# Kernel optimization log

Measured on AMD Instinct MI355X. Metric: run time of the kernel, lower is better.

The kernel has to match this reference:

```python
import jax, jax.numpy as jnp
import numpy as np

N_HEADS = 16
D_K = 64
D_V = 64
HIDDEN = 1024
B, S = 2, 2048
LN_EPS = 1e-5


def setup_inputs() -> dict:
    key = jax.random.key(0)
    ks = jax.random.split(key, 6)
    inputs = jax.random.normal(ks[0], (B, S, HIDDEN), dtype=jnp.float32)
    attn_mask = jax.random.randint(ks[1], (B, S, S), 0, 2, dtype=jnp.int32)
    scale = 1.0 / np.sqrt(HIDDEN)
    W_Q = jax.random.normal(ks[2], (HIDDEN, HIDDEN), dtype=jnp.float32) * scale
    W_K = jax.random.normal(ks[3], (HIDDEN, HIDDEN), dtype=jnp.float32) * scale
    W_V = jax.random.normal(ks[4], (HIDDEN, HIDDEN), dtype=jnp.float32) * scale
    W_O = jax.random.normal(ks[5], (HIDDEN, HIDDEN), dtype=jnp.float32) * scale
    return {"inputs": inputs, "attn_mask": attn_mask,
            "W_Q": W_Q, "W_K": W_K, "W_V": W_V, "W_O": W_O}


def reference(inputs, attn_mask, W_Q, W_K, W_V, W_O):
    b, s, _ = inputs.shape
    # nn.Linear(bias=False): x @ W.T ; reshape to [B, H, S, d]
    Q = (inputs @ W_Q.T).reshape(b, s, N_HEADS, D_K).transpose(0, 2, 1, 3)
    K = (inputs @ W_K.T).reshape(b, s, N_HEADS, D_K).transpose(0, 2, 1, 3)
    V = (inputs @ W_V.T).reshape(b, s, N_HEADS, D_V).transpose(0, 2, 1, 3)
    scores = jnp.einsum('bhqd,bhkd->bhqk', Q, K) / np.sqrt(D_K)
    mask = (attn_mask == 0)[:, None, :, :]  # broadcast over heads
    scores = jnp.where(mask, jnp.float32(-1e9), scores)
    attn = jax.nn.softmax(scores, axis=-1)
    context = jnp.einsum('bhqk,bhkd->bhqd', attn, V)
    context = context.transpose(0, 2, 1, 3).reshape(b, s, N_HEADS * D_V)
    output = context @ W_O.T
    x = output + inputs  # residual
    # LayerNorm with default weight=1, bias=0, eps=1e-5
    mu = jnp.mean(x, axis=-1, keepdims=True)
    var = jnp.mean(jnp.square(x - mu), axis=-1, keepdims=True)
    out = (x - mu) * jax.lax.rsqrt(var + LN_EPS)
    return out, attn
```

## Files before the change

kernel.cpp:

```cpp
#include <hip/hip_runtime.h>

typedef unsigned short u16;
typedef __bf16 bf16x8 __attribute__((ext_vector_type(8)));
typedef float f32x4 __attribute__((ext_vector_type(4)));

static __device__ __forceinline__ u16 f32_to_bf16(float f) {
    unsigned u = __builtin_bit_cast(unsigned, f);
    u += 0x7fffu + ((u >> 16) & 1u);
    return (u16)(u >> 16);
}
static __device__ __forceinline__ float bf16_to_f32(u16 v) {
    return __builtin_bit_cast(float, ((unsigned)v) << 16);
}

__global__ __launch_bounds__(256) void cast_f32_bf16(const float* __restrict__ in,
                                                     u16* __restrict__ out, int n)
{
    int i = (blockIdx.x * 256 + threadIdx.x) * 4;
    if (i >= n) return;
    float4 v = *reinterpret_cast<const float4*>(in + i);
    ushort4 o;
    o.x = f32_to_bf16(v.x); o.y = f32_to_bf16(v.y);
    o.z = f32_to_bf16(v.z); o.w = f32_to_bf16(v.w);
    *reinterpret_cast<ushort4*>(out + i) = o;
}

__global__ __launch_bounds__(256) void gemm_abt_bf16(
    const u16* __restrict__ A, const u16* __restrict__ B,
    u16* __restrict__ C, int M, int N, int K)
{
    __shared__ __align__(16) u16 As[64][40];
    __shared__ __align__(16) u16 Bs[64][40];
    const int tid  = threadIdx.x;
    const int wave = tid >> 6, lane = tid & 63;
    const int quad = lane >> 4, l16 = lane & 15;
    const int m0 = blockIdx.y * 64, n0 = blockIdx.x * 64;

    f32x4 acc[4] = {};
    const int lr = tid >> 2;
    const int lc = (tid & 3) * 8;
    const u16* Ap = A + (size_t)(m0 + lr) * K + lc;
    const u16* Bp = B + (size_t)(n0 + lr) * K + lc;

    for (int k0 = 0; k0 < K; k0 += 32) {
        __syncthreads();
        *reinterpret_cast<int4*>(&As[lr][lc]) = *reinterpret_cast<const int4*>(Ap + k0);
        *reinterpret_cast<int4*>(&Bs[lr][lc]) = *reinterpret_cast<const int4*>(Bp + k0);
        __syncthreads();
        bf16x8 a = *reinterpret_cast<const bf16x8*>(&As[wave * 16 + l16][quad * 8]);
#pragma unroll
        for (int cb = 0; cb < 4; ++cb) {
            bf16x8 b = *reinterpret_cast<const bf16x8*>(&Bs[cb * 16 + l16][quad * 8]);
            acc[cb] = __builtin_amdgcn_mfma_f32_16x16x32_bf16(a, b, acc[cb], 0, 0, 0);
        }
    }
#pragma unroll
    for (int cb = 0; cb < 4; ++cb)
#pragma unroll
        for (int r = 0; r < 4; ++r) {
            int row = m0 + wave * 16 + quad * 4 + r;
            int col = n0 + cb * 16 + l16;
            C[(size_t)row * N + col] = f32_to_bf16(acc[cb][r]);
        }
}

__global__ __launch_bounds__(256) void gemm_abt_res_f32(
    const u16* __restrict__ A, const u16* __restrict__ B,
    const float* __restrict__ X, float* __restrict__ C, int M, int N, int K)
{
    __shared__ __align__(16) u16 As[64][40];
    __shared__ __align__(16) u16 Bs[64][40];
    const int tid  = threadIdx.x;
    const int wave = tid >> 6, lane = tid & 63;
    const int quad = lane >> 4, l16 = lane & 15;
    const int m0 = blockIdx.y * 64, n0 = blockIdx.x * 64;

    f32x4 acc[4] = {};
    const int lr = tid >> 2;
    const int lc = (tid & 3) * 8;
    const u16* Ap = A + (size_t)(m0 + lr) * K + lc;
    const u16* Bp = B + (size_t)(n0 + lr) * K + lc;

    for (int k0 = 0; k0 < K; k0 += 32) {
        __syncthreads();
        *reinterpret_cast<int4*>(&As[lr][lc]) = *reinterpret_cast<const int4*>(Ap + k0);
        *reinterpret_cast<int4*>(&Bs[lr][lc]) = *reinterpret_cast<const int4*>(Bp + k0);
        __syncthreads();
        bf16x8 a = *reinterpret_cast<const bf16x8*>(&As[wave * 16 + l16][quad * 8]);
#pragma unroll
        for (int cb = 0; cb < 4; ++cb) {
            bf16x8 b = *reinterpret_cast<const bf16x8*>(&Bs[cb * 16 + l16][quad * 8]);
            acc[cb] = __builtin_amdgcn_mfma_f32_16x16x32_bf16(a, b, acc[cb], 0, 0, 0);
        }
    }
#pragma unroll
    for (int cb = 0; cb < 4; ++cb)
#pragma unroll
        for (int r = 0; r < 4; ++r) {
            int row = m0 + wave * 16 + quad * 4 + r;
            int col = n0 + cb * 16 + l16;
            C[(size_t)row * N + col] = acc[cb][r] + X[(size_t)row * N + col];
        }
}

__global__ __launch_bounds__(256) void attn_kernel(
    const u16* __restrict__ Q, const u16* __restrict__ K,
    const u16* __restrict__ V, const int* __restrict__ mask,
    float* __restrict__ attn_out, u16* __restrict__ ctx_out)
{
    constexpr int S = 2048, HID = 1024, NH = 16;
    __shared__ __align__(16) u16 Qs[64][72];
    __shared__ __align__(16) u16 Ks[64][72];
    __shared__ __align__(16) u16 Vt[64][72];
    __shared__ __align__(16) u16 Ps[64][72];

    const int tid  = threadIdx.x;
    const int wave = tid >> 6, lane = tid & 63;
    const int quad = lane >> 4, l16 = lane & 15;
    const int qt = blockIdx.x, h = blockIdx.y, b = blockIdx.z;
    const size_t qkv_base = (size_t)b * S * HID + h * 64;

    const int lr = tid >> 2;
    const int lc = (tid & 3) * 16;
    {
        const u16* p = Q + qkv_base + (size_t)(qt * 64 + lr) * HID + lc;
        *reinterpret_cast<int4*>(&Qs[lr][lc])     = *reinterpret_cast<const int4*>(p);
        *reinterpret_cast<int4*>(&Qs[lr][lc + 8]) = *reinterpret_cast<const int4*>(p + 8);
    }

    float m_i[4], l_i[4];
#pragma unroll
    for (int r = 0; r < 4; ++r) { m_i[r] = -1e30f; l_i[r] = 0.f; }

    const int q_row0 = qt * 64 + wave * 16 + quad * 4;
    const size_t mask_b = (size_t)b * S * S;

    for (int kt = 0; kt < S / 64; ++kt) {
        __syncthreads();
        {
            const u16* p = K + qkv_base + (size_t)(kt * 64 + lr) * HID + lc;
            *reinterpret_cast<int4*>(&Ks[lr][lc])     = *reinterpret_cast<const int4*>(p);
            *reinterpret_cast<int4*>(&Ks[lr][lc + 8]) = *reinterpret_cast<const int4*>(p + 8);
        }
        __syncthreads();
        f32x4 sc[4] = {};
#pragma unroll
        for (int ks = 0; ks < 2; ++ks) {
            bf16x8 a = *reinterpret_cast<const bf16x8*>(&Qs[wave * 16 + l16][ks * 32 + quad * 8]);
#pragma unroll
            for (int cb = 0; cb < 4; ++cb) {
                bf16x8 bb = *reinterpret_cast<const bf16x8*>(&Ks[cb * 16 + l16][ks * 32 + quad * 8]);
                sc[cb] = __builtin_amdgcn_mfma_f32_16x16x32_bf16(a, bb, sc[cb], 0, 0, 0);
            }
        }
        float s_val[4][4];
#pragma unroll
        for (int cb = 0; cb < 4; ++cb) {
            int kcol = kt * 64 + cb * 16 + l16;
#pragma unroll
            for (int r = 0; r < 4; ++r) {
                int q = q_row0 + r;
                int mv = mask[mask_b + (size_t)q * S + kcol];
                s_val[cb][r] = (mv == 0) ? -1e9f : sc[cb][r] * 0.125f;
            }
        }
#pragma unroll
        for (int r = 0; r < 4; ++r) {
            float mx = fmaxf(fmaxf(s_val[0][r], s_val[1][r]), fmaxf(s_val[2][r], s_val[3][r]));
            mx = fmaxf(mx, __shfl_xor(mx, 1));
            mx = fmaxf(mx, __shfl_xor(mx, 2));
            mx = fmaxf(mx, __shfl_xor(mx, 4));
            mx = fmaxf(mx, __shfl_xor(mx, 8));
            float m_new = fmaxf(m_i[r], mx);
            float sum = 0.f;
#pragma unroll
            for (int cb = 0; cb < 4; ++cb) sum += __expf(s_val[cb][r] - m_new);
            sum += __shfl_xor(sum, 1);
            sum += __shfl_xor(sum, 2);
            sum += __shfl_xor(sum, 4);
            sum += __shfl_xor(sum, 8);
            l_i[r] = l_i[r] * __expf(m_i[r] - m_new) + sum;
            m_i[r] = m_new;
        }
    }
    float rl[4];
#pragma unroll
    for (int r = 0; r < 4; ++r) rl[r] = 1.0f / l_i[r];

    f32x4 ctx[4] = {};
    for (int kt = 0; kt < S / 64; ++kt) {
        __syncthreads();
        {
            const u16* p = K + qkv_base + (size_t)(kt * 64 + lr) * HID + lc;
            *reinterpret_cast<int4*>(&Ks[lr][lc])     = *reinterpret_cast<const int4*>(p);
            *reinterpret_cast<int4*>(&Ks[lr][lc + 8]) = *reinterpret_cast<const int4*>(p + 8);
            const u16* pv = V + qkv_base + (size_t)(kt * 64 + lr) * HID + lc;
            union { int4 v; u16 s[8]; } b0, b1;
            b0.v = *reinterpret_cast<const int4*>(pv);
            b1.v = *reinterpret_cast<const int4*>(pv + 8);
#pragma unroll
            for (int j = 0; j < 8; ++j) Vt[lc + j][lr] = b0.s[j];
#pragma unroll
            for (int j = 0; j < 8; ++j) Vt[lc + 8 + j][lr] = b1.s[j];
        }
        __syncthreads();
        f32x4 sc[4] = {};
#pragma unroll
        for (int ks = 0; ks < 2; ++ks) {
            bf16x8 a = *reinterpret_cast<const bf16x8*>(&Qs[wave * 16 + l16][ks * 32 + quad * 8]);
#pragma unroll
            for (int cb = 0; cb < 4; ++cb) {
                bf16x8 bb = *reinterpret_cast<const bf16x8*>(&Ks[cb * 16 + l16][ks * 32 + quad * 8]);
                sc[cb] = __builtin_amdgcn_mfma_f32_16x16x32_bf16(a, bb, sc[cb], 0, 0, 0);
            }
        }
#pragma unroll
        for (int cb = 0; cb < 4; ++cb) {
            int kcol = kt * 64 + cb * 16 + l16;
#pragma unroll
            for (int r = 0; r < 4; ++r) {
                int q = q_row0 + r;
                int mv = mask[mask_b + (size_t)q * S + kcol];
                float s = (mv == 0) ? -1e9f : sc[cb][r] * 0.125f;
                float pval = __expf(s - m_i[r]) * rl[r];
                Ps[wave * 16 + quad * 4 + r][cb * 16 + l16] = f32_to_bf16(pval);
            }
        }
        __syncthreads();
        {
            size_t arow = (((size_t)(b * NH + h) * S) + qt * 64 + lr) * S + kt * 64 + lc;
#pragma unroll
            for (int g = 0; g < 4; ++g) {
                float4 o;
                o.x = bf16_to_f32(Ps[lr][lc + g * 4 + 0]);
                o.y = bf16_to_f32(Ps[lr][lc + g * 4 + 1]);
                o.z = bf16_to_f32(Ps[lr][lc + g * 4 + 2]);
                o.w = bf16_to_f32(Ps[lr][lc + g * 4 + 3]);
                *reinterpret_cast<float4*>(&attn_out[arow + g * 4]) = o;
            }
        }
#pragma unroll
        for (int ks = 0; ks < 2; ++ks) {
            bf16x8 a = *reinterpret_cast<const bf16x8*>(&Ps[wave * 16 + l16][ks * 32 + quad * 8]);
#pragma unroll
            for (int cb = 0; cb < 4; ++cb) {
                bf16x8 bb = *reinterpret_cast<const bf16x8*>(&Vt[cb * 16 + l16][ks * 32 + quad * 8]);
                ctx[cb] = __builtin_amdgcn_mfma_f32_16x16x32_bf16(a, bb, ctx[cb], 0, 0, 0);
            }
        }
    }
#pragma unroll
    for (int cb = 0; cb < 4; ++cb)
#pragma unroll
        for (int r = 0; r < 4; ++r) {
            int q = q_row0 + r;
            int d = cb * 16 + l16;
            ctx_out[qkv_base + (size_t)q * HID + d] = f32_to_bf16(ctx[cb][r]);
        }
}

__global__ __launch_bounds__(256) void ln_kernel(const float* __restrict__ X,
                                                 float* __restrict__ out)
{
    __shared__ float red[8];
    const int row = blockIdx.x;
    const int tid = threadIdx.x;
    const int wave = tid >> 6, lane = tid & 63;
    const float* xr = X + (size_t)row * 1024;
    float v[4];
    float s = 0.f;
#pragma unroll
    for (int i = 0; i < 4; ++i) { v[i] = xr[tid + 256 * i]; s += v[i]; }
#pragma unroll
    for (int off = 1; off < 64; off <<= 1) s += __shfl_xor(s, off);
    if (lane == 0) red[wave] = s;
    __syncthreads();
    float mean = (red[0] + red[1] + red[2] + red[3]) * (1.0f / 1024.0f);
    float s2 = 0.f;
#pragma unroll
    for (int i = 0; i < 4; ++i) { float d = v[i] - mean; s2 += d * d; }
#pragma unroll
    for (int off = 1; off < 64; off <<= 1) s2 += __shfl_xor(s2, off);
    if (lane == 0) red[4 + wave] = s2;
    __syncthreads();
    float var = (red[4] + red[5] + red[6] + red[7]) * (1.0f / 1024.0f);
    float rstd = rsqrtf(var + 1e-5f);
#pragma unroll
    for (int i = 0; i < 4; ++i)
        out[(size_t)row * 1024 + tid + 256 * i] = (v[i] - mean) * rstd;
}

extern "C" void kernel_launch(void* const* d_in, const int* in_sizes, int n_in,
                              void* d_out, int out_size, void* d_ws, size_t ws_size,
                              hipStream_t stream)
{
    constexpr int B = 2, S = 2048, HID = 1024, NH = 16;
    constexpr int M = B * S;

    const float* X  = (const float*)d_in[0];
    const int* mask = (const int*)d_in[1];
    const float* WQ = (const float*)d_in[2];
    const float* WK = (const float*)d_in[3];
    const float* WV = (const float*)d_in[4];
    const float* WO = (const float*)d_in[5];

    float* out  = (float*)d_out;
    float* attn = out + (size_t)M * HID;

    u16*   Xb  = (u16*)d_ws;
    u16*   WQb = Xb  + (size_t)M * HID;
    u16*   WKb = WQb + (size_t)HID * HID;
    u16*   WVb = WKb + (size_t)HID * HID;
    u16*   WOb = WVb + (size_t)HID * HID;
    u16*   Qw  = WOb + (size_t)HID * HID;
    u16*   Kw  = Qw  + (size_t)M * HID;
    u16*   Vw  = Kw  + (size_t)M * HID;
    u16*   Cw  = Vw  + (size_t)M * HID;
    float* XO  = (float*)(Cw + (size_t)M * HID);

    dim3 blk(256);
    cast_f32_bf16<<<dim3((M * HID) / 1024), blk, 0, stream>>>(X,  Xb,  M * HID);
    cast_f32_bf16<<<dim3((HID * HID) / 1024), blk, 0, stream>>>(WQ, WQb, HID * HID);
    cast_f32_bf16<<<dim3((HID * HID) / 1024), blk, 0, stream>>>(WK, WKb, HID * HID);
    cast_f32_bf16<<<dim3((HID * HID) / 1024), blk, 0, stream>>>(WV, WVb, HID * HID);
    cast_f32_bf16<<<dim3((HID * HID) / 1024), blk, 0, stream>>>(WO, WOb, HID * HID);

    dim3 ggrid(HID / 64, M / 64);
    gemm_abt_bf16<<<ggrid, blk, 0, stream>>>(Xb, WQb, Qw, M, HID, HID);
    gemm_abt_bf16<<<ggrid, blk, 0, stream>>>(Xb, WKb, Kw, M, HID, HID);
    gemm_abt_bf16<<<ggrid, blk, 0, stream>>>(Xb, WVb, Vw, M, HID, HID);

    dim3 agrid(S / 64, NH, B);
    attn_kernel<<<agrid, blk, 0, stream>>>(Qw, Kw, Vw, mask, attn, Cw);

    gemm_abt_res_f32<<<ggrid, blk, 0, stream>>>(Cw, WOb, X, XO, M, HID, HID);
    ln_kernel<<<dim3(M), blk, 0, stream>>>(XO, out);
}
```

Baseline: 915.1 us.

## Bit-pack mask, use 128x128 fused QKV GEMM, pre-transpose V, merge weight casts

New measurement: 889.3 us. -2.8%, faster.

```diff
diff --git a/kernel.cpp b/kernel.cpp
--- a/kernel.cpp
+++ b/kernel.cpp
@@ -1,6 +1,7 @@
 #include <hip/hip_runtime.h>
 
 typedef unsigned short u16;
+typedef unsigned long long u64;
 typedef __bf16 bf16x8 __attribute__((ext_vector_type(8)));
 typedef float f32x4 __attribute__((ext_vector_type(4)));
 
@@ -25,93 +26,198 @@
     *reinterpret_cast<ushort4*>(out + i) = o;
 }
 
-__global__ __launch_bounds__(256) void gemm_abt_bf16(
-    const u16* __restrict__ A, const u16* __restrict__ B,
-    u16* __restrict__ C, int M, int N, int K)
-{
-    __shared__ __align__(16) u16 As[64][40];
-    __shared__ __align__(16) u16 Bs[64][40];
+__global__ __launch_bounds__(256) void cast_w4(
+    const float* __restrict__ w0, const float* __restrict__ w1,
+    const float* __restrict__ w2, const float* __restrict__ w3,
+    u16* __restrict__ o0, u16* __restrict__ o1,
+    u16* __restrict__ o2, u16* __restrict__ o3)
+{
+    const float* src; u16* dst;
+    switch (blockIdx.y) {
+        case 0: src = w0; dst = o0; break;
+        case 1: src = w1; dst = o1; break;
+        case 2: src = w2; dst = o2; break;
+        default: src = w3; dst = o3; break;
+    }
+    int i = (blockIdx.x * 256 + threadIdx.x) * 4;
+    float4 v = *reinterpret_cast<const float4*>(src + i);
+    ushort4 o;
+    o.x = f32_to_bf16(v.x); o.y = f32_to_bf16(v.y);
+    o.z = f32_to_bf16(v.z); o.w = f32_to_bf16(v.w);
+    *reinterpret_cast<ushort4*>(dst + i) = o;
+}
+
+__global__ __launch_bounds__(256) void pack_mask(const int* __restrict__ mask,
+                                                 u64* __restrict__ out)
+{
+    int t = blockIdx.x * 256 + threadIdx.x;
+    const int4* p = reinterpret_cast<const int4*>(mask + (size_t)t * 64);
+    u64 bits = 0;
+#pragma unroll
+    for (int j = 0; j < 16; ++j) {
+        int4 v = p[j];
+        bits |= ((u64)(v.x != 0)) << (j * 4 + 0);
+        bits |= ((u64)(v.y != 0)) << (j * 4 + 1);
+        bits |= ((u64)(v.z != 0)) << (j * 4 + 2);
+        bits |= ((u64)(v.w != 0)) << (j * 4 + 3);
+    }
+    out[t] = bits;
+}
+
+__global__ __launch_bounds__(256) void gemm128_qkv(
+    const u16* __restrict__ A,
+    const u16* __restrict__ BQ, const u16* __restrict__ BK, const u16* __restrict__ BV,
+    u16* __restrict__ CQ, u16* __restrict__ CK, u16* __restrict__ CV)
+{
+    constexpr int N = 1024, K = 1024;
+    const u16* B; u16* C;
+    switch (blockIdx.z) {
+        case 0:  B = BQ; C = CQ; break;
+        case 1:  B = BK; C = CK; break;
+        default: B = BV; C = CV; break;
+    }
+    __shared__ __align__(16) u16 As[128][72];
+    __shared__ __align__(16) u16 Bs[128][72];
     const int tid  = threadIdx.x;
     const int wave = tid >> 6, lane = tid & 63;
     const int quad = lane >> 4, l16 = lane & 15;
-    const int m0 = blockIdx.y * 64, n0 = blockIdx.x * 64;
-
-    f32x4 acc[4] = {};
-    const int lr = tid >> 2;
-    const int lc = (tid & 3) * 8;
-    const u16* Ap = A + (size_t)(m0 + lr) * K + lc;
-    const u16* Bp = B + (size_t)(n0 + lr) * K + lc;
-
-    for (int k0 = 0; k0 < K; k0 += 32) {
-        __syncthreads();
-        *reinterpret_cast<int4*>(&As[lr][lc]) = *reinterpret_cast<const int4*>(Ap + k0);
-        *reinterpret_cast<int4*>(&Bs[lr][lc]) = *reinterpret_cast<const int4*>(Bp + k0);
-        __syncthreads();
-        bf16x8 a = *reinterpret_cast<const bf16x8*>(&As[wave * 16 + l16][quad * 8]);
-#pragma unroll
-        for (int cb = 0; cb < 4; ++cb) {
-            bf16x8 b = *reinterpret_cast<const bf16x8*>(&Bs[cb * 16 + l16][quad * 8]);
-            acc[cb] = __builtin_amdgcn_mfma_f32_16x16x32_bf16(a, b, acc[cb], 0, 0, 0);
-        }
-    }
-#pragma unroll
-    for (int cb = 0; cb < 4; ++cb)
-#pragma unroll
-        for (int r = 0; r < 4; ++r) {
-            int row = m0 + wave * 16 + quad * 4 + r;
-            int col = n0 + cb * 16 + l16;
-            C[(size_t)row * N + col] = f32_to_bf16(acc[cb][r]);
-        }
-}
-
-__global__ __launch_bounds__(256) void gemm_abt_res_f32(
+    const int wr = wave >> 1, wc = wave & 1;
+    const int m0 = blockIdx.y * 128, n0 = blockIdx.x * 128;
+
+    f32x4 acc[4][4] = {};
+    const int r0 = tid >> 3;
+    const int c0 = (tid & 7) * 8;
+    const u16* Ap = A + (size_t)(m0 + r0) * K + c0;
+    const u16* Bp = B + (size_t)(n0 + r0) * K + c0;
+
+    for (int k0 = 0; k0 < K; k0 += 64) {
+        __syncthreads();
+#pragma unroll
+        for (int i = 0; i < 4; ++i) {
+            *reinterpret_cast<int4*>(&As[r0 + 32 * i][c0]) =
+                *reinterpret_cast<const int4*>(Ap + (size_t)(32 * i) * K + k0);
+            *reinterpret_cast<int4*>(&Bs[r0 + 32 * i][c0]) =
+                *reinterpret_cast<const int4*>(Bp + (size_t)(32 * i) * K + k0);
+        }
+        __syncthreads();
+#pragma unroll
+        for (int ks = 0; ks < 2; ++ks) {
+            bf16x8 a[4], bb[4];
+#pragma unroll
+            for (int mi = 0; mi < 4; ++mi)
+                a[mi] = *reinterpret_cast<const bf16x8*>(&As[wr * 64 + mi * 16 + l16][ks * 32 + quad * 8]);
+#pragma unroll
+            for (int ni = 0; ni < 4; ++ni)
+                bb[ni] = *reinterpret_cast<const bf16x8*>(&Bs[wc * 64 + ni * 16 + l16][ks * 32 + quad * 8]);
+#pragma unroll
+            for (int mi = 0; mi < 4; ++mi)
+#pragma unroll
+                for (int ni = 0; ni < 4; ++ni)
+                    acc[mi][ni] = __builtin_amdgcn_mfma_f32_16x16x32_bf16(a[mi], bb[ni], acc[mi][ni], 0, 0, 0);
+        }
+    }
+#pragma unroll
+    for (int mi = 0; mi < 4; ++mi)
+#pragma unroll
+        for (int ni = 0; ni < 4; ++ni)
+#pragma unroll
+            for (int r = 0; r < 4; ++r) {
+                int row = m0 + wr * 64 + mi * 16 + quad * 4 + r;
+                int col = n0 + wc * 64 + ni * 16 + l16;
+                C[(size_t)row * N + col] = f32_to_bf16(acc[mi][ni][r]);
+            }
+}
+
+__global__ __launch_bounds__(256) void gemm128_res(
     const u16* __restrict__ A, const u16* __restrict__ B,
-    const float* __restrict__ X, float* __restrict__ C, int M, int N, int K)
-{
-    __shared__ __align__(16) u16 As[64][40];
-    __shared__ __align__(16) u16 Bs[64][40];
+    const float* __restrict__ X, float* __restrict__ C)
+{
+    constexpr int N = 1024, K = 1024;
+    __shared__ __align__(16) u16 As[128][72];
+    __shared__ __align__(16) u16 Bs[128][72];
     const int tid  = threadIdx.x;
     const int wave = tid >> 6, lane = tid & 63;
     const int quad = lane >> 4, l16 = lane & 15;
-    const int m0 = blockIdx.y * 64, n0 = blockIdx.x * 64;
-
-    f32x4 acc[4] = {};
-    const int lr = tid >> 2;
-    const int lc = (tid & 3) * 8;
-    const u16* Ap = A + (size_t)(m0 + lr) * K + lc;
-    const u16* Bp = B + (size_t)(n0 + lr) * K + lc;
-
-    for (int k0 = 0; k0 < K; k0 += 32) {
-        __syncthreads();
-        *reinterpret_cast<int4*>(&As[lr][lc]) = *reinterpret_cast<const int4*>(Ap + k0);
-        *reinterpret_cast<int4*>(&Bs[lr][lc]) = *reinterpret_cast<const int4*>(Bp + k0);
-        __syncthreads();
-        bf16x8 a = *reinterpret_cast<const bf16x8*>(&As[wave * 16 + l16][quad * 8]);
-#pragma unroll
-        for (int cb = 0; cb < 4; ++cb) {
-            bf16x8 b = *reinterpret_cast<const bf16x8*>(&Bs[cb * 16 + l16][quad * 8]);
-            acc[cb] = __builtin_amdgcn_mfma_f32_16x16x32_bf16(a, b, acc[cb], 0, 0, 0);
-        }
-    }
-#pragma unroll
-    for (int cb = 0; cb < 4; ++cb)
-#pragma unroll
-        for (int r = 0; r < 4; ++r) {
-            int row = m0 + wave * 16 + quad * 4 + r;
-            int col = n0 + cb * 16 + l16;
-            C[(size_t)row * N + col] = acc[cb][r] + X[(size_t)row * N + col];
-        }
+    const int wr = wave >> 1, wc = wave & 1;
+    const int m0 = blockIdx.y * 128, n0 = blockIdx.x * 128;
+
+    f32x4 acc[4][4] = {};
+    const int r0 = tid >> 3;
+    const int c0 = (tid & 7) * 8;
+    const u16* Ap = A + (size_t)(m0 + r0) * K + c0;
+    const u16* Bp = B + (size_t)(n0 + r0) * K + c0;
+
+    for (int k0 = 0; k0 < K; k0 += 64) {
+        __syncthreads();
+#pragma unroll
+        for (int i = 0; i < 4; ++i) {
+            *reinterpret_cast<int4*>(&As[r0 + 32 * i][c0]) =
+                *reinterpret_cast<const int4*>(Ap + (size_t)(32 * i) * K + k0);
+            *reinterpret_cast<int4*>(&Bs[r0 + 32 * i][c0]) =
+                *reinterpret_cast<const int4*>(Bp + (size_t)(32 * i) * K + k0);
+        }
+        __syncthreads();
+#pragma unroll
+        for (int ks = 0; ks < 2; ++ks) {
+            bf16x8 a[4], bb[4];
+#pragma unroll
+            for (int mi = 0; mi < 4; ++mi)
+                a[mi] = *reinterpret_cast<const bf16x8*>(&As[wr * 64 + mi * 16 + l16][ks * 32 + quad * 8]);
+#pragma unroll
+            for (int ni = 0; ni < 4; ++ni)
+                bb[ni] = *reinterpret_cast<const bf16x8*>(&Bs[wc * 64 + ni * 16 + l16][ks * 32 + quad * 8]);
+#pragma unroll
+            for (int mi = 0; mi < 4; ++mi)
+#pragma unroll
+                for (int ni = 0; ni < 4; ++ni)
+                    acc[mi][ni] = __builtin_amdgcn_mfma_f32_16x16x32_bf16(a[mi], bb[ni], acc[mi][ni], 0, 0, 0);
+        }
+    }
+#pragma unroll
+    for (int mi = 0; mi < 4; ++mi)
+#pragma unroll
+        for (int ni = 0; ni < 4; ++ni)
+#pragma unroll
+            for (int r = 0; r < 4; ++r) {
+                int row = m0 + wr * 64 + mi * 16 + quad * 4 + r;
+                int col = n0 + wc * 64 + ni * 16 + l16;
+                C[(size_t)row * N + col] = acc[mi][ni][r] + X[(size_t)row * N + col];
+            }
+}
+
+__global__ __launch_bounds__(256) void transpose_v(const u16* __restrict__ Vw,
+                                                   u16* __restrict__ VT)
+{
+    constexpr int S = 2048, HID = 1024, NH = 16;
+    __shared__ __align__(16) u16 Ts[64][72];
+    const int tid = threadIdx.x;
+    const int lr = tid >> 2, lc = (tid & 3) * 16;
+    const int st = blockIdx.x, h = blockIdx.y, b = blockIdx.z;
+    {
+        const u16* p = Vw + ((size_t)(b * S + st * 64 + lr)) * HID + h * 64 + lc;
+        *reinterpret_cast<int4*>(&Ts[lr][lc])     = *reinterpret_cast<const int4*>(p);
+        *reinterpret_cast<int4*>(&Ts[lr][lc + 8]) = *reinterpret_cast<const int4*>(p + 8);
+    }
+    __syncthreads();
+    u16* q = VT + ((size_t)((b * NH + h) * 64 + lr)) * S + st * 64 + lc;
+    union { int4 v; u16 s[8]; } o0, o1;
+#pragma unroll
+    for (int j = 0; j < 8; ++j) o0.s[j] = Ts[lc + j][lr];
+#pragma unroll
+    for (int j = 0; j < 8; ++j) o1.s[j] = Ts[lc + 8 + j][lr];
+    *reinterpret_cast<int4*>(q)     = o0.v;
+    *reinterpret_cast<int4*>(q + 8) = o1.v;
 }
 
 __global__ __launch_bounds__(256) void attn_kernel(
     const u16* __restrict__ Q, const u16* __restrict__ K,
-    const u16* __restrict__ V, const int* __restrict__ mask,
+    const u16* __restrict__ VT, const u64* __restrict__ Mb,
     float* __restrict__ attn_out, u16* __restrict__ ctx_out)
 {
     constexpr int S = 2048, HID = 1024, NH = 16;
     __shared__ __align__(16) u16 Qs[64][72];
     __shared__ __align__(16) u16 Ks[64][72];
-    __shared__ __align__(16) u16 Vt[64][72];
+    __shared__ __align__(16) u16 Vs[64][72];
     __shared__ __align__(16) u16 Ps[64][72];
 
     const int tid  = threadIdx.x;
@@ -119,6 +225,7 @@
     const int quad = lane >> 4, l16 = lane & 15;
     const int qt = blockIdx.x, h = blockIdx.y, b = blockIdx.z;
     const size_t qkv_base = (size_t)b * S * HID + h * 64;
+    const size_t vt_base  = ((size_t)(b * NH + h)) * 64 * S;
 
     const int lr = tid >> 2;
     const int lc = (tid & 3) * 16;
@@ -133,9 +240,12 @@
     for (int r = 0; r < 4; ++r) { m_i[r] = -1e30f; l_i[r] = 0.f; }
 
     const int q_row0 = qt * 64 + wave * 16 + quad * 4;
-    const size_t mask_b = (size_t)b * S * S;
+    const size_t mrow = (size_t)b * S + q_row0;
 
     for (int kt = 0; kt < S / 64; ++kt) {
+        u64 mw[4];
+#pragma unroll
+        for (int r = 0; r < 4; ++r) mw[r] = Mb[(mrow + r) * 32 + kt];
         __syncthreads();
         {
             const u16* p = K + qkv_base + (size_t)(kt * 64 + lr) * HID + lc;
@@ -156,13 +266,10 @@
         float s_val[4][4];
 #pragma unroll
         for (int cb = 0; cb < 4; ++cb) {
-            int kcol = kt * 64 + cb * 16 + l16;
-#pragma unroll
-            for (int r = 0; r < 4; ++r) {
-                int q = q_row0 + r;
-                int mv = mask[mask_b + (size_t)q * S + kcol];
-                s_val[cb][r] = (mv == 0) ? -1e9f : sc[cb][r] * 0.125f;
-            }
+            int bi = cb * 16 + l16;
+#pragma unroll
+            for (int r = 0; r < 4; ++r)
+                s_val[cb][r] = ((mw[r] >> bi) & 1ull) ? sc[cb][r] * 0.125f : -1e9f;
         }
 #pragma unroll
         for (int r = 0; r < 4; ++r) {
@@ -189,19 +296,17 @@
 
     f32x4 ctx[4] = {};
     for (int kt = 0; kt < S / 64; ++kt) {
+        u64 mw[4];
+#pragma unroll
+        for (int r = 0; r < 4; ++r) mw[r] = Mb[(mrow + r) * 32 + kt];
         __syncthreads();
         {
             const u16* p = K + qkv_base + (size_t)(kt * 64 + lr) * HID + lc;
             *reinterpret_cast<int4*>(&Ks[lr][lc])     = *reinterpret_cast<const int4*>(p);
             *reinterpret_cast<int4*>(&Ks[lr][lc + 8]) = *reinterpret_cast<const int4*>(p + 8);
-            const u16* pv = V + qkv_base + (size_t)(kt * 64 + lr) * HID + lc;
-            union { int4 v; u16 s[8]; } b0, b1;
-            b0.v = *reinterpret_cast<const int4*>(pv);
-            b1.v = *reinterpret_cast<const int4*>(pv + 8);
-#pragma unroll
-            for (int j = 0; j < 8; ++j) Vt[lc + j][lr] = b0.s[j];
-#pragma unroll
-            for (int j = 0; j < 8; ++j) Vt[lc + 8 + j][lr] = b1.s[j];
+            const u16* pv = VT + vt_base + (size_t)lr * S + kt * 64 + lc;
+            *reinterpret_cast<int4*>(&Vs[lr][lc])     = *reinterpret_cast<const int4*>(pv);
+            *reinterpret_cast<int4*>(&Vs[lr][lc + 8]) = *reinterpret_cast<const int4*>(pv + 8);
         }
         __syncthreads();
         f32x4 sc[4] = {};
@@ -216,12 +321,10 @@
         }
 #pragma unroll
         for (int cb = 0; cb < 4; ++cb) {
-            int kcol = kt * 64 + cb * 16 + l16;
+            int bi = cb * 16 + l16;
 #pragma unroll
             for (int r = 0; r < 4; ++r) {
-                int q = q_row0 + r;
-                int mv = mask[mask_b + (size_t)q * S + kcol];
-                float s = (mv == 0) ? -1e9f : sc[cb][r] * 0.125f;
+                float s = ((mw[r] >> bi) & 1ull) ? sc[cb][r] * 0.125f : -1e9f;
                 float pval = __expf(s - m_i[r]) * rl[r];
                 Ps[wave * 16 + quad * 4 + r][cb * 16 + l16] = f32_to_bf16(pval);
             }
@@ -244,7 +347,7 @@
             bf16x8 a = *reinterpret_cast<const bf16x8*>(&Ps[wave * 16 + l16][ks * 32 + quad * 8]);
 #pragma unroll
             for (int cb = 0; cb < 4; ++cb) {
-                bf16x8 bb = *reinterpret_cast<const bf16x8*>(&Vt[cb * 16 + l16][ks * 32 + quad * 8]);
+                bf16x8 bb = *reinterpret_cast<const bf16x8*>(&Vs[cb * 16 + l16][ks * 32 + quad * 8]);
                 ctx[cb] = __builtin_amdgcn_mfma_f32_16x16x32_bf16(a, bb, ctx[cb], 0, 0, 0);
             }
         }
@@ -307,7 +410,8 @@
     float* out  = (float*)d_out;
     float* attn = out + (size_t)M * HID;
 
-    u16*   Xb  = (u16*)d_ws;
+    u64*   Mb  = (u64*)d_ws;
+    u16*   Xb  = (u16*)(Mb + (size_t)B * S * 32);
     u16*   WQb = Xb  + (size_t)M * HID;
     u16*   WKb = WQb + (size_t)HID * HID;
     u16*   WVb = WKb + (size_t)HID * HID;
@@ -316,23 +420,21 @@
     u16*   Kw  = Qw  + (size_t)M * HID;
     u16*   Vw  = Kw  + (size_t)M * HID;
     u16*   Cw  = Vw  + (size_t)M * HID;
-    float* XO  = (float*)(Cw + (size_t)M * HID);
+    u16*   VT  = Xb;
+    float* XO  = (float*)Qw;
 
     dim3 blk(256);
-    cast_f32_bf16<<<dim3((M * HID) / 1024), blk, 0, stream>>>(X,  Xb,  M * HID);
-    cast_f32_bf16<<<dim3((HID * HID) / 1024), blk, 0, stream>>>(WQ, WQb, HID * HID);
-    cast_f32_bf16<<<dim3((HID * HID) / 1024), blk, 0, stream>>>(WK, WKb, HID * HID);
-    cast_f32_bf16<<<dim3((HID * HID) / 1024), blk, 0, stream>>>(WV, WVb, HID * HID);
-    cast_f32_bf16<<<dim3((HID * HID) / 1024), blk, 0, stream>>>(WO, WOb, HID * HID);
-
-    dim3 ggrid(HID / 64, M / 64);
-    gemm_abt_bf16<<<ggrid, blk, 0, stream>>>(Xb, WQb, Qw, M, HID, HID);
-    gemm_abt_bf16<<<ggrid, blk, 0, stream>>>(Xb, WKb, Kw, M, HID, HID);
-    gemm_abt_bf16<<<ggrid, blk, 0, stream>>>(Xb, WVb, Vw, M, HID, HID);
-
-    dim3 agrid(S / 64, NH, B);
-    attn_kernel<<<agrid, blk, 0, stream>>>(Qw, Kw, Vw, mask, attn, Cw);
-
-    gemm_abt_res_f32<<<ggrid, blk, 0, stream>>>(Cw, WOb, X, XO, M, HID, HID);
+    cast_f32_bf16<<<dim3((M * HID) / 1024), blk, 0, stream>>>(X, Xb, M * HID);
+    cast_w4<<<dim3((HID * HID) / 1024, 4), blk, 0, stream>>>(WQ, WK, WV, WO,
+                                                             WQb, WKb, WVb, WOb);
+    pack_mask<<<dim3((B * S * 32) / 256), blk, 0, stream>>>(mask, Mb);
+
+    gemm128_qkv<<<dim3(HID / 128, M / 128, 3), blk, 0, stream>>>(Xb, WQb, WKb, WVb,
+                                                                 Qw, Kw, Vw);
+    transpose_v<<<dim3(S / 64, NH, B), blk, 0, stream>>>(Vw, VT);
+
+    attn_kernel<<<dim3(S / 64, NH, B), blk, 0, stream>>>(Qw, Kw, VT, Mb, attn, Cw);
+
+    gemm128_res<<<dim3(HID / 128, M / 128), blk, 0, stream>>>(Cw, WOb, X, XO);
     ln_kernel<<<dim3(M), blk, 0, stream>>>(XO, out);
 }
```
